# Kernel optimization log

Hardware: AMD Instinct MI355X
Metric: run time of the kernel (lower is better)

Reference implementation:

```python
import jax, jax.numpy as jnp
import numpy as np

B, S, E, H, L = 32, 1024, 768, 64, 2  # batch, seq (<=1024 per bias buffer), embed, head hidden, labels
MASKED_BIAS = jnp.float32(-10000.0)


def setup_inputs() -> dict:
    key = jax.random.key(0)
    ks = jax.random.split(key, 12)
    s = 0.02  # init scale
    return {
        "hidden": jax.random.normal(ks[0], (B, S, E), dtype=jnp.float32),
        "attention_mask": jnp.ones((B, S), dtype=jnp.float32),
        # torch nn.Linear weights are [out, in]
        "Wk": jax.random.normal(ks[1], (E, E), dtype=jnp.float32) * s,
        "bk": jnp.zeros((E,), dtype=jnp.float32),
        "Wq": jax.random.normal(ks[2], (E, E), dtype=jnp.float32) * s,
        "bq": jnp.zeros((E,), dtype=jnp.float32),
        "Wv": jax.random.normal(ks[3], (E, E), dtype=jnp.float32) * s,
        "bv": jnp.zeros((E,), dtype=jnp.float32),
        "W1": jax.random.normal(ks[4], (H, E), dtype=jnp.float32) * s,
        "b1": jnp.zeros((H,), dtype=jnp.float32),
        "W2": jax.random.normal(ks[5], (L, H), dtype=jnp.float32) * s,
        "b2": jnp.zeros((L,), dtype=jnp.float32),
    }


def reference(hidden, attention_mask, Wk, bk, Wq, bq, Wv, bv, W1, b1, W2, b2):
    # Single-head causal attention, NO 1/sqrt(d) scaling (faithful to source).
    # Dropout layers run in eval mode -> identity.
    seq = hidden.shape[1]
    q = hidden @ Wq.T + bq            # [B,S,E]
    k = hidden @ Wk.T + bk            # [B,S,E]
    v = hidden @ Wv.T + bv            # [B,S,E] (v_drop is identity in eval)
    w = jnp.einsum('bqe,bke->bqk', q, k)  # [B,S,S]
    causal = jnp.tril(jnp.ones((seq, seq), dtype=bool))  # bias[:, ns-nd:ns, :ns] with nd==ns
    w = jnp.where(causal, w, MASKED_BIAS.astype(w.dtype))
    am = (1.0 - attention_mask)[:, None, :] * -10000.0    # [B,1,S]
    w = jax.nn.softmax(w + am, axis=-1)
    h = jnp.einsum('bqk,bke->bqe', w, v)  # [B,S,E]
    h = jax.nn.relu(h @ W1.T + b1)        # [B,S,64]
    return h @ W2.T + b2                  # [B,S,L]
```

## Files before the change

kernel.cpp:

```cpp
#include <hip/hip_runtime.h>
#include <hip/hip_bf16.h>
#include <cstdio>


typedef _Float16 f16;
typedef f16    f16x8 __attribute__((ext_vector_type(8)));
typedef f16    f16x4 __attribute__((ext_vector_type(4)));
typedef __bf16 bfx8  __attribute__((ext_vector_type(8)));
typedef float  f32x4 __attribute__((ext_vector_type(4)));

#define MFMA_F16(a,b,c)  __builtin_amdgcn_mfma_f32_16x16x32_f16((a),(b),(c),0,0,0)
#define MFMA_BF16(a,b,c) __builtin_amdgcn_mfma_f32_16x16x32_bf16((a),(b),(c),0,0,0)

static constexpr int LDT2 = 264;

__device__ __forceinline__ void gl_lds16(const void* g, void* l) {
    __builtin_amdgcn_global_load_lds(
        (const __attribute__((address_space(1))) void*)g,
        (__attribute__((address_space(3))) void*)l, 16, 0, 0);
}

#define WAIT_VMCNT(n)                                        \
    do { asm volatile("s_waitcnt vmcnt(" #n ")");            \
         __builtin_amdgcn_sched_barrier(0); } while (0)
#define WAIT_LGKM0()                                         \
    do { asm volatile("s_waitcnt lgkmcnt(0)");               \
         __builtin_amdgcn_sched_barrier(0); } while (0)

__global__ __launch_bounds__(256) void cvt_all(
    const float* __restrict__ hidden,
    const float* __restrict__ Wq, const float* __restrict__ Wk, const float* __restrict__ Wv,
    f16* __restrict__ h16, f16* __restrict__ oq, f16* __restrict__ ok, f16* __restrict__ ov)
{
    const int bid = blockIdx.x;
    const float* src;
    f16* dst;
    int base;
    if (bid < 24576) {
        src = hidden; dst = h16;
        base = (bid * 256 + threadIdx.x) * 4;
    } else {
        int wz = (bid - 24576) / 576, wb = (bid - 24576) % 576;
        src = (wz == 0) ? Wq : (wz == 1) ? Wk : Wv;
        dst = (wz == 0) ? oq : (wz == 1) ? ok : ov;
        base = (wb * 256 + threadIdx.x) * 4;
    }
    f32x4 v = *(const f32x4*)(src + base);
    f16x4 o;
    #pragma unroll
    for (int e = 0; e < 4; ++e) o[e] = (f16)v[e];
    *(f16x4*)(dst + base) = o;
}

#define QPHASE(fr0, STAGE_STMT, GATE_STMT)                                        \
    {                                                                             \
        f16x8 afr[2][2];                                                          \
        _Pragma("unroll")                                                         \
        for (int i = 0; i < 2; ++i) {                                             \
            _Pragma("unroll")                                                     \
            for (int kk = 0; kk < 2; ++kk)                                        \
                afr[i][kk] = *(const f16x8*)&SA[kk * 8192 + (wr8 + (fr0) + i) * 512 + lq]; \
        }                                                                         \
        STAGE_STMT;                                                               \
        GATE_STMT;                                                                \
        __builtin_amdgcn_s_barrier();                                             \
        WAIT_LGKM0();                                                             \
        __builtin_amdgcn_s_setprio(1);                                            \
        _Pragma("unroll")                                                         \
        for (int i = 0; i < 2; ++i) {                                             \
            _Pragma("unroll")                                                     \
            for (int jj = 0; jj < 4; ++jj) {                                      \
                acc[(fr0) + i][jj] = MFMA_F16(afr[i][0], bfr[jj][0], acc[(fr0) + i][jj]); \
                acc[(fr0) + i][jj] = MFMA_F16(afr[i][1], bfr[jj][1], acc[(fr0) + i][jj]); \
            }                                                                     \
        }                                                                         \
        __builtin_amdgcn_s_setprio(0);                                            \
        __builtin_amdgcn_s_barrier();                                             \
    }

#define QPHASE_BF(fr0, STAGE_STMT, GATE_STMT)                                     \
    {                                                                             \
        bfx8 afr[2][2];                                                           \
        _Pragma("unroll")                                                         \
        for (int i = 0; i < 2; ++i) {                                             \
            _Pragma("unroll")                                                     \
            for (int kk = 0; kk < 2; ++kk)                                        \
                afr[i][kk] = *(const bfx8*)&SA[kk * 8192 + (wr8 + (fr0) + i) * 512 + lq]; \
        }                                                                         \
        STAGE_STMT;                                                               \
        GATE_STMT;                                                                \
        __builtin_amdgcn_s_barrier();                                             \
        WAIT_LGKM0();                                                             \
        __builtin_amdgcn_s_setprio(1);                                            \
        _Pragma("unroll")                                                         \
        for (int i = 0; i < 2; ++i) {                                             \
            _Pragma("unroll")                                                     \
            for (int jj = 0; jj < 4; ++jj) {                                      \
                acc[(fr0) + i][jj] = MFMA_BF16(afr[i][0], bfr[jj][0], acc[(fr0) + i][jj]); \
                acc[(fr0) + i][jj] = MFMA_BF16(afr[i][1], bfr[jj][1], acc[(fr0) + i][jj]); \
            }                                                                     \
        }                                                                         \
        __builtin_amdgcn_s_setprio(0);                                            \
        __builtin_amdgcn_s_barrier();                                             \
    }

__global__ __launch_bounds__(512, 2) void qkv_kernel(
    const f16* __restrict__ h16,
    const f16* __restrict__ wq, const f16* __restrict__ wk, const f16* __restrict__ wv,
    const float* __restrict__ bq, const float* __restrict__ bk, const float* __restrict__ bv,
    f16* __restrict__ q16, f16* __restrict__ k16, __bf16* __restrict__ vT)
{
    const int f = blockIdx.x;
    const int xcd = f & 7;
    const int j = f >> 3;
    const int nt = j % 3;
    const int z  = (j / 3) % 3;
    const int mi = j / 9;
    const int mt = xcd + 8 * mi;
    const int m0 = mt * 256, n0 = nt * 256;

    const f16* W = (z == 0) ? wq : (z == 1) ? wk : wv;
    const float* bias = (z == 0) ? bq : (z == 1) ? bk : bv;

    __shared__ alignas(16) f16 S[65536];

    const int t = threadIdx.x, lane = t & 63, wave = t >> 6;
    const int wr = wave >> 2, wc = wave & 3;
    const int wr8 = wr * 8;
    const int quad = lane >> 4, l16 = lane & 15;
    const int lq = quad * 128 + l16 * 8;

    const f16* gA = h16 + (size_t)(m0 + l16) * 768 + quad * 8;
    const f16* gB = W   + (size_t)(n0 + l16) * 768 + quad * 8;
    int gofs[2], lofs[2];
    #pragma unroll
    for (int u = 0; u < 2; ++u) {
        int unit = wave * 2 + u;
        int kk = unit >> 3, c = unit & 7;
        gofs[u] = c * 16 * 768 + kk * 32;
        lofs[u] = kk * 8192 + c * 512;
    }
    auto stage = [&](int kt, int mat, int half) {
        const f16* gp = (mat ? gB : gA) + half * (128 * 768) + kt * 64;
        f16* lp = &S[(kt & 1) * 32768 + mat * 16384 + half * 4096];
        gl_lds16(gp + gofs[0], lp + lofs[0]);
        gl_lds16(gp + gofs[1], lp + lofs[1]);
    };

    f32x4 acc[8][4] = {};

    stage(0, 0, 0); stage(0, 0, 1); stage(0, 1, 0); stage(0, 1, 1);
    stage(1, 1, 0); stage(1, 1, 1);
    WAIT_VMCNT(4);
    __builtin_amdgcn_s_barrier();

    f16x8 bfr[4][2];
    for (int kt = 0; kt < 12; ++kt) {
        const f16* SA = &S[(kt & 1) * 32768];
        const f16* SB = SA + 16384;
        #pragma unroll
        for (int jj = 0; jj < 4; ++jj) {
            #pragma unroll
            for (int kk = 0; kk < 2; ++kk)
                bfr[jj][kk] = *(const f16x8*)&SB[kk * 8192 + (wc * 4 + jj) * 512 + lq];
        }
        QPHASE(0, { if (kt + 1 < 12) stage(kt + 1, 0, 0); }, {});
        QPHASE(2, { if (kt + 1 < 12) stage(kt + 1, 0, 1); }, {});
        QPHASE(4, { if (kt + 2 < 12) stage(kt + 2, 1, 0); }, {});
        QPHASE(6, { if (kt + 2 < 12) stage(kt + 2, 1, 1); },
               {
                   if (kt + 2 < 12)       WAIT_VMCNT(4);
                   else if (kt + 1 < 12)  WAIT_VMCNT(0);
               });
    }

    if (z < 2) {
        f16* out = z ? k16 : q16;
        #pragma unroll
        for (int jj = 0; jj < 4; ++jj) {
            int col = n0 + wc * 64 + jj * 16 + l16;
            float bb = bias[col];
            #pragma unroll
            for (int fi = 0; fi < 8; ++fi) {
                #pragma unroll
                for (int r = 0; r < 4; ++r) {
                    int row = m0 + wr * 128 + fi * 16 + quad * 4 + r;
                    out[(size_t)row * 768 + col] = (f16)(acc[fi][jj][r] + bb);
                }
            }
        }
    } else {
        __bf16* Tb = (__bf16*)S;
        const int halfw = wc >> 1;
        const int bofs = (m0 >> 10) * 768;
        const int s0 = m0 & 1023;
        #pragma unroll
        for (int half = 0; half < 2; ++half) {
            __syncthreads();
            if (halfw == half) {
                #pragma unroll
                for (int jj = 0; jj < 4; ++jj) {
                    int el = (wc & 1) * 64 + jj * 16 + l16;
                    float bb = bias[n0 + half * 128 + el];
                    #pragma unroll
                    for (int fi = 0; fi < 8; ++fi) {
                        #pragma unroll
                        for (int r = 0; r < 4; ++r) {
                            int sl = wr * 128 + fi * 16 + quad * 4 + r;
                            Tb[el * LDT2 + sl] = (__bf16)(acc[fi][jj][r] + bb);
                        }
                    }
                }
            }
            __syncthreads();
            const int ch = (t & 31) * 8;
            const int rbase = t >> 5;
            #pragma unroll
            for (int p = 0; p < 8; ++p) {
                int e = rbase + p * 16;
                bfx8 val = *(const bfx8*)&Tb[e * LDT2 + ch];
                *(bfx8*)&vT[(size_t)(bofs + n0 + half * 128 + e) * 1024 + s0 + ch] = val;
            }
        }
    }
}

__global__ __launch_bounds__(512, 2) void logits_kernel(
    const f16* __restrict__ q16, const f16* __restrict__ k16,
    const float* __restrict__ amask, __bf16* __restrict__ pu, float* __restrict__ psum)
{
    const int f = blockIdx.x;
    const int xcd = f & 7;
    const int j = f >> 3;
    const int b = xcd + 8 * (j / 10);
    const int tile = j % 10;
    int mt, nt;
    if (tile < 4)      { mt = 3; nt = tile; }
    else if (tile < 7) { mt = 2; nt = tile - 4; }
    else if (tile < 9) { mt = 1; nt = tile - 7; }
    else               { mt = 0; nt = 0; }
    const int m0 = mt * 256, n0 = nt * 256;
    const size_t pb = (size_t)b << 20;
    const size_t qb = (size_t)b * 1024 * 768;

    __shared__ alignas(16) f16 S[65536];
    __shared__ float rs[4][256];

    const int t = threadIdx.x, lane = t & 63, wave = t >> 6;
    const int wr = wave >> 2, wc = wave & 3;
    const int wr8 = wr * 8;
    const int quad = lane >> 4, l16 = lane & 15;
    const int lq = quad * 128 + l16 * 8;

    const f16* gA = q16 + qb + (size_t)(m0 + l16) * 768 + quad * 8;
    const f16* gB = k16 + qb + (size_t)(n0 + l16) * 768 + quad * 8;
    int gofs[2], lofs[2];
    #pragma unroll
    for (int u = 0; u < 2; ++u) {
        int unit = wave * 2 + u;
        int kk = unit >> 3, c = unit & 7;
        gofs[u] = c * 16 * 768 + kk * 32;
        lofs[u] = kk * 8192 + c * 512;
    }
    auto stage = [&](int kt, int mat, int half) {
        const f16* gp = (mat ? gB : gA) + half * (128 * 768) + kt * 64;
        f16* lp = &S[(kt & 1) * 32768 + mat * 16384 + half * 4096];
        gl_lds16(gp + gofs[0], lp + lofs[0]);
        gl_lds16(gp + gofs[1], lp + lofs[1]);
    };

    f32x4 acc[8][4] = {};

    stage(0, 0, 0); stage(0, 0, 1); stage(0, 1, 0); stage(0, 1, 1);
    stage(1, 1, 0); stage(1, 1, 1);
    WAIT_VMCNT(4);
    __builtin_amdgcn_s_barrier();

    f16x8 bfr[4][2];
    for (int kt = 0; kt < 12; ++kt) {
        const f16* SA = &S[(kt & 1) * 32768];
        const f16* SB = SA + 16384;
        #pragma unroll
        for (int jj = 0; jj < 4; ++jj) {
            #pragma unroll
            for (int kk = 0; kk < 2; ++kk)
                bfr[jj][kk] = *(const f16x8*)&SB[kk * 8192 + (wc * 4 + jj) * 512 + lq];
        }
        QPHASE(0, { if (kt + 1 < 12) stage(kt + 1, 0, 0); }, {});
        QPHASE(2, { if (kt + 1 < 12) stage(kt + 1, 0, 1); }, {});
        QPHASE(4, { if (kt + 2 < 12) stage(kt + 2, 1, 0); }, {});
        QPHASE(6, { if (kt + 2 < 12) stage(kt + 2, 1, 1); },
               {
                   if (kt + 2 < 12)       WAIT_VMCNT(4);
                   else if (kt + 1 < 12)  WAIT_VMCNT(0);
               });
    }

    float rp[8][4] = {};
    #pragma unroll
    for (int jj = 0; jj < 4; ++jj) {
        int col = n0 + wc * 64 + jj * 16 + l16;
        float am = (1.0f - amask[b * 1024 + col]) * -10000.0f;
        #pragma unroll
        for (int fi = 0; fi < 8; ++fi) {
            #pragma unroll
            for (int r = 0; r < 4; ++r) {
                int row = m0 + wr * 128 + fi * 16 + quad * 4 + r;
                float s = acc[fi][jj][r] + am;
                float pval = (col <= row) ? __expf(fminf(s, 80.0f)) : 0.0f;
                pu[pb + (size_t)row * 1024 + col] = (__bf16)pval;
                rp[fi][r] += pval;
            }
        }
    }
    #pragma unroll
    for (int fi = 0; fi < 8; ++fi) {
        #pragma unroll
        for (int r = 0; r < 4; ++r) {
            float v = rp[fi][r];
            v += __shfl_xor(v, 1, 64);
            v += __shfl_xor(v, 2, 64);
            v += __shfl_xor(v, 4, 64);
            v += __shfl_xor(v, 8, 64);
            if (l16 == 0) rs[wc][wr * 128 + fi * 16 + quad * 4 + r] = v;
        }
    }
    __syncthreads();
    if (t < 256)
        psum[((size_t)b * 1024 + m0 + t) * 4 + nt] =
            rs[0][t] + rs[1][t] + rs[2][t] + rs[3][t];
}

__global__ __launch_bounds__(512, 2) void pv_kernel(
    const __bf16* __restrict__ pu, const __bf16* __restrict__ vT,
    const float* __restrict__ psum, __bf16* __restrict__ h)
{
    const int f = blockIdx.x;
    const int xcd = f & 7;
    const int j = f >> 3;
    const int b = xcd + 8 * (j / 12);
    const int tile = j % 12;
    const int mt = 3 - tile / 3, nt = tile % 3;
    const int m0 = mt * 256, n0 = nt * 256;
    const int nkt = 4 * (mt + 1);
    const size_t pb = (size_t)b << 20;
    const size_t vb = (size_t)b * 768 * 1024;

    __shared__ alignas(16) __bf16 S[65536];
    __shared__ float invl[256];

    const int t = threadIdx.x, lane = t & 63, wave = t >> 6;
    const int wr = wave >> 2, wc = wave & 3;
    const int wr8 = wr * 8;
    const int quad = lane >> 4, l16 = lane & 15;
    const int lq = quad * 128 + l16 * 8;

    if (t < 256) {
        int row = m0 + t;
        int lim = row >> 8;
        const float* pr = &psum[((size_t)b * 1024 + row) * 4];
        float s = 0.f;
        #pragma unroll
        for (int n = 0; n < 4; ++n) s += (n <= lim) ? pr[n] : 0.f;
        invl[t] = 1.0f / s;
    }

    const __bf16* gA = pu + pb + (size_t)(m0 + l16) * 1024 + quad * 8;
    const __bf16* gB = vT + vb + (size_t)(n0 + l16) * 1024 + quad * 8;
    int gofs[2], lofs[2];
    #pragma unroll
    for (int u = 0; u < 2; ++u) {
        int unit = wave * 2 + u;
        int kk = unit >> 3, c = unit & 7;
        gofs[u] = c * 16 * 1024 + kk * 32;
        lofs[u] = kk * 8192 + c * 512;
    }
    auto stage = [&](int kt, int mat, int half) {
        const __bf16* gp = (mat ? gB : gA) + half * (128 * 1024) + kt * 64;
        __bf16* lp = &S[(kt & 1) * 32768 + mat * 16384 + half * 4096];
        gl_lds16(gp + gofs[0], lp + lofs[0]);
        gl_lds16(gp + gofs[1], lp + lofs[1]);
    };

    f32x4 acc[8][4] = {};

    stage(0, 0, 0); stage(0, 0, 1); stage(0, 1, 0); stage(0, 1, 1);
    stage(1, 1, 0); stage(1, 1, 1);
    WAIT_VMCNT(4);
    __builtin_amdgcn_s_barrier();

    bfx8 bfr[4][2];
    for (int kt = 0; kt < nkt; ++kt) {
        const __bf16* SA = &S[(kt & 1) * 32768];
        const __bf16* SB = SA + 16384;
        #pragma unroll
        for (int jj = 0; jj < 4; ++jj) {
            #pragma unroll
            for (int kk = 0; kk < 2; ++kk)
                bfr[jj][kk] = *(const bfx8*)&SB[kk * 8192 + (wc * 4 + jj) * 512 + lq];
        }
        QPHASE_BF(0, { if (kt + 1 < nkt) stage(kt + 1, 0, 0); }, {});
        QPHASE_BF(2, { if (kt + 1 < nkt) stage(kt + 1, 0, 1); }, {});
        QPHASE_BF(4, { if (kt + 2 < nkt) stage(kt + 2, 1, 0); }, {});
        QPHASE_BF(6, { if (kt + 2 < nkt) stage(kt + 2, 1, 1); },
               {
                   if (kt + 2 < nkt)       WAIT_VMCNT(4);
                   else if (kt + 1 < nkt)  WAIT_VMCNT(0);
               });
    }

    #pragma unroll
    for (int jj = 0; jj < 4; ++jj) {
        int col = n0 + wc * 64 + jj * 16 + l16;
        #pragma unroll
        for (int fi = 0; fi < 8; ++fi) {
            #pragma unroll
            for (int r = 0; r < 4; ++r) {
                int rl = wr * 128 + fi * 16 + quad * 4 + r;
                h[((size_t)b * 1024 + m0 + rl) * 768 + col] = (__bf16)(acc[fi][jj][r] * invl[rl]);
            }
        }
    }
}

__global__ __launch_bounds__(256) void mlp_kernel(
    const __bf16* __restrict__ h, const float* __restrict__ W1, const float* __restrict__ b1,
    const float* __restrict__ W2, const float* __restrict__ b2, float* __restrict__ out)
{
    const int wave = threadIdx.x >> 6, lane = threadIdx.x & 63;
    const int quad = lane >> 4, l16 = lane & 15;
    const int m0 = blockIdx.x * 64 + wave * 16;

    f32x4 acc[4] = {};
    for (int k0 = 0; k0 < 768; k0 += 32) {
        bfx8 af = *(const bfx8*)&h[(size_t)(m0 + l16) * 768 + k0 + quad * 8];
        #pragma unroll
        for (int jj = 0; jj < 4; ++jj) {
            const float* wp = W1 + (size_t)(jj * 16 + l16) * 768 + k0 + quad * 8;
            f32x4 w0 = *(const f32x4*)wp;
            f32x4 w1 = *(const f32x4*)(wp + 4);
            bfx8 bg;
            #pragma unroll
            for (int e = 0; e < 4; ++e) { bg[e] = (__bf16)w0[e]; bg[e + 4] = (__bf16)w1[e]; }
            acc[jj] = MFMA_BF16(af, bg, acc[jj]);
        }
    }
    float part[4][2] = {};
    #pragma unroll
    for (int jj = 0; jj < 4; ++jj) {
        int c = jj * 16 + l16;
        float bb = b1[c];
        float w20 = W2[c], w21 = W2[64 + c];
        #pragma unroll
        for (int r = 0; r < 4; ++r) {
            float x = fmaxf(acc[jj][r] + bb, 0.f);
            part[r][0] += x * w20;
            part[r][1] += x * w21;
        }
    }
    #pragma unroll
    for (int off = 1; off < 16; off <<= 1)
        #pragma unroll
        for (int r = 0; r < 4; ++r) {
            part[r][0] += __shfl_xor(part[r][0], off, 64);
            part[r][1] += __shfl_xor(part[r][1], off, 64);
        }
    if (l16 == 0) {
        #pragma unroll
        for (int r = 0; r < 4; ++r) {
            int row = m0 + quad * 4 + r;
            out[(size_t)row * 2 + 0] = part[r][0] + b2[0];
            out[(size_t)row * 2 + 1] = part[r][1] + b2[1];
        }
    }
}

extern "C" void kernel_launch(void* const* d_in, const int* in_sizes, int n_in,
                              void* d_out, int out_size, void* d_ws, size_t ws_size,
                              hipStream_t stream)
{
    const float* hidden = (const float*)d_in[0];
    const float* amask  = (const float*)d_in[1];
    const float* Wk = (const float*)d_in[2];
    const float* bk = (const float*)d_in[3];
    const float* Wq = (const float*)d_in[4];
    const float* bq = (const float*)d_in[5];
    const float* Wv = (const float*)d_in[6];
    const float* bv = (const float*)d_in[7];
    const float* W1 = (const float*)d_in[8];
    const float* b1 = (const float*)d_in[9];
    const float* W2 = (const float*)d_in[10];
    const float* b2 = (const float*)d_in[11];
    float* out = (float*)d_out;

    char* ws = (char*)d_ws;
    const size_t MB = 1024 * 1024;
    f16* h16 = (f16*)ws;
    f16* wq16 = (f16*)(ws + 48 * MB);
    f16* wk16 = wq16 + 589824;
    f16* wv16 = wk16 + 589824;
    __bf16* pu  = (__bf16*)ws;
    float*  psum = (float*)(ws + 64 * MB);
    f16* q16 = (f16*)(ws + 66 * MB);
    f16* k16 = (f16*)(ws + 114 * MB);
    __bf16* vT = (__bf16*)(ws + 162 * MB);
    __bf16* h  = (__bf16*)(ws + 66 * MB);
    const size_t NEED = 210 * MB;
    if (ws_size < NEED) {
        fprintf(stderr, "[Attn kernel] ws too small: %zu < %zu — skipping launches\n",
                ws_size, NEED);
        return;
    }

    cvt_all<<<24576 + 1728, 256, 0, stream>>>(
        hidden, Wq, Wk, Wv, h16, wq16, wk16, wv16);

    qkv_kernel<<<1152, 512, 0, stream>>>(
        h16, wq16, wk16, wv16, bq, bk, bv, q16, k16, vT);
    logits_kernel<<<320, 512, 0, stream>>>(q16, k16, amask, pu, psum);
    pv_kernel<<<384, 512, 0, stream>>>(pu, vT, psum, h);
    mlp_kernel<<<512, 256, 0, stream>>>(h, W1, b1, W2, b2, out);
}
```

Measured before the change: 519.5 us.

## Replace direct global-to-LDS loads with register-staged prefetch in all GEMM kernels

```diff
diff --git a/kernel.cpp b/kernel.cpp
--- a/kernel.cpp
+++ b/kernel.cpp
@@ -8,23 +8,16 @@
 typedef f16    f16x4 __attribute__((ext_vector_type(4)));
 typedef __bf16 bfx8  __attribute__((ext_vector_type(8)));
 typedef float  f32x4 __attribute__((ext_vector_type(4)));
+typedef unsigned int u32;
+typedef u32    u32x4 __attribute__((ext_vector_type(4)));
 
 #define MFMA_F16(a,b,c)  __builtin_amdgcn_mfma_f32_16x16x32_f16((a),(b),(c),0,0,0)
 #define MFMA_BF16(a,b,c) __builtin_amdgcn_mfma_f32_16x16x32_bf16((a),(b),(c),0,0,0)
 
 static constexpr int LDT2 = 264;
 
-__device__ __forceinline__ void gl_lds16(const void* g, void* l) {
-    __builtin_amdgcn_global_load_lds(
-        (const __attribute__((address_space(1))) void*)g,
-        (__attribute__((address_space(3))) void*)l, 16, 0, 0);
-}
-
-#define WAIT_VMCNT(n)                                        \
-    do { asm volatile("s_waitcnt vmcnt(" #n ")");            \
-         __builtin_amdgcn_sched_barrier(0); } while (0)
-#define WAIT_LGKM0()                                         \
-    do { asm volatile("s_waitcnt lgkmcnt(0)");               \
+#define PUB()                                                \
+    do { asm volatile("s_waitcnt lgkmcnt(0)" ::: "memory");  \
          __builtin_amdgcn_sched_barrier(0); } while (0)
 
 __global__ __launch_bounds__(256) void cvt_all(
@@ -52,19 +45,19 @@
     *(f16x4*)(dst + base) = o;
 }
 
-#define QPHASE(fr0, STAGE_STMT, GATE_STMT)                                        \
+#define QPHASE(fr0, ST_STMT, LD_STMT)                                             \
     {                                                                             \
         f16x8 afr[2][2];                                                          \
         _Pragma("unroll")                                                         \
         for (int i = 0; i < 2; ++i) {                                             \
             _Pragma("unroll")                                                     \
-            for (int kk = 0; kk < 2; ++kk)                                        \
-                afr[i][kk] = *(const f16x8*)&SA[kk * 8192 + (wr8 + (fr0) + i) * 512 + lq]; \
+            for (int kk2 = 0; kk2 < 2; ++kk2)                                     \
+                afr[i][kk2] = *(const f16x8*)&SA[kk2 * 8192 + (wr8 + (fr0) + i) * 512 + lq]; \
         }                                                                         \
-        STAGE_STMT;                                                               \
-        GATE_STMT;                                                                \
+        ST_STMT;                                                                  \
+        LD_STMT;                                                                  \
+        PUB();                                                                    \
         __builtin_amdgcn_s_barrier();                                             \
-        WAIT_LGKM0();                                                             \
         __builtin_amdgcn_s_setprio(1);                                            \
         _Pragma("unroll")                                                         \
         for (int i = 0; i < 2; ++i) {                                             \
@@ -78,19 +71,19 @@
         __builtin_amdgcn_s_barrier();                                             \
     }
 
-#define QPHASE_BF(fr0, STAGE_STMT, GATE_STMT)                                     \
+#define QPHASE_BF(fr0, ST_STMT, LD_STMT)                                          \
     {                                                                             \
         bfx8 afr[2][2];                                                           \
         _Pragma("unroll")                                                         \
         for (int i = 0; i < 2; ++i) {                                             \
             _Pragma("unroll")                                                     \
-            for (int kk = 0; kk < 2; ++kk)                                        \
-                afr[i][kk] = *(const bfx8*)&SA[kk * 8192 + (wr8 + (fr0) + i) * 512 + lq]; \
+            for (int kk2 = 0; kk2 < 2; ++kk2)                                     \
+                afr[i][kk2] = *(const bfx8*)&SA[kk2 * 8192 + (wr8 + (fr0) + i) * 512 + lq]; \
         }                                                                         \
-        STAGE_STMT;                                                               \
-        GATE_STMT;                                                                \
+        ST_STMT;                                                                  \
+        LD_STMT;                                                                  \
+        PUB();                                                                    \
         __builtin_amdgcn_s_barrier();                                             \
-        WAIT_LGKM0();                                                             \
         __builtin_amdgcn_s_setprio(1);                                            \
         _Pragma("unroll")                                                         \
         for (int i = 0; i < 2; ++i) {                                             \
@@ -103,6 +96,15 @@
         __builtin_amdgcn_s_setprio(0);                                            \
         __builtin_amdgcn_s_barrier();                                             \
     }
+
+#define LD2(s_a, s_b, GP)                                    \
+    do { const char* _g = (const char*)(GP);                 \
+         s_a = *(const u32x4*)_g;                            \
+         s_b = *(const u32x4*)(_g + GO1B); } while (0)
+#define ST2(s_a, s_b, LP)                                    \
+    do { char* _l = (char*)(LP);                             \
+         *(u32x4*)_l = s_a;                                  \
+         *(u32x4*)(_l + 1024) = s_b; } while (0)
 
 __global__ __launch_bounds__(512, 2) void qkv_kernel(
     const f16* __restrict__ h16,
@@ -130,29 +132,34 @@
     const int quad = lane >> 4, l16 = lane & 15;
     const int lq = quad * 128 + l16 * 8;
 
-    const f16* gA = h16 + (size_t)(m0 + l16) * 768 + quad * 8;
-    const f16* gB = W   + (size_t)(n0 + l16) * 768 + quad * 8;
-    int gofs[2], lofs[2];
-    #pragma unroll
-    for (int u = 0; u < 2; ++u) {
-        int unit = wave * 2 + u;
-        int kk = unit >> 3, c = unit & 7;
-        gofs[u] = c * 16 * 768 + kk * 32;
-        lofs[u] = kk * 8192 + c * 512;
-    }
-    auto stage = [&](int kt, int mat, int half) {
-        const f16* gp = (mat ? gB : gA) + half * (128 * 768) + kt * 64;
-        f16* lp = &S[(kt & 1) * 32768 + mat * 16384 + half * 4096];
-        gl_lds16(gp + gofs[0], lp + lofs[0]);
-        gl_lds16(gp + gofs[1], lp + lofs[1]);
+    enum { GO1B = 16 * 768 * 2, HOFF = 128 * 768 };
+    const int c0 = (wave * 2) & 7, kk0 = wave >> 2;
+    const int gofs0 = c0 * 16 * 768 + kk0 * 32;
+    const int lofs0 = kk0 * 8192 + c0 * 512 + lane * 8;
+
+    const f16* gA = h16 + (size_t)(m0 + l16) * 768 + quad * 8 + gofs0;
+    const f16* gB = W   + (size_t)(n0 + l16) * 768 + quad * 8 + gofs0;
+    auto gp = [&](int mat, int kt, int half) {
+        return (mat ? gB : gA) + half * HOFF + kt * 64;
     };
+    auto lp = [&](int kt, int mat, int half) {
+        return &S[(kt & 1) * 32768 + mat * 16384 + half * 4096 + lofs0];
+    };
 
     f32x4 acc[8][4] = {};
-
-    stage(0, 0, 0); stage(0, 0, 1); stage(0, 1, 0); stage(0, 1, 1);
-    stage(1, 1, 0); stage(1, 1, 1);
-    WAIT_VMCNT(4);
-    __builtin_amdgcn_s_barrier();
+    u32x4 sA0a, sA0b, sA1a, sA1b, sB0a, sB0b, sB1a, sB1b;
+
+    {
+        u32x4 p0a, p0b, p1a, p1b, p2a, p2b, p3a, p3b, p4a, p4b, p5a, p5b;
+        LD2(p0a, p0b, gp(0, 0, 0)); LD2(p1a, p1b, gp(0, 0, 1));
+        LD2(p2a, p2b, gp(1, 0, 0)); LD2(p3a, p3b, gp(1, 0, 1));
+        LD2(p4a, p4b, gp(1, 1, 0)); LD2(p5a, p5b, gp(1, 1, 1));
+        ST2(p0a, p0b, lp(0, 0, 0)); ST2(p1a, p1b, lp(0, 0, 1));
+        ST2(p2a, p2b, lp(0, 1, 0)); ST2(p3a, p3b, lp(0, 1, 1));
+        ST2(p4a, p4b, lp(1, 1, 0)); ST2(p5a, p5b, lp(1, 1, 1));
+        PUB();
+        __builtin_amdgcn_s_barrier();
+    }
 
     f16x8 bfr[4][2];
     for (int kt = 0; kt < 12; ++kt) {
@@ -161,17 +168,17 @@
         #pragma unroll
         for (int jj = 0; jj < 4; ++jj) {
             #pragma unroll
-            for (int kk = 0; kk < 2; ++kk)
-                bfr[jj][kk] = *(const f16x8*)&SB[kk * 8192 + (wc * 4 + jj) * 512 + lq];
-        }
-        QPHASE(0, { if (kt + 1 < 12) stage(kt + 1, 0, 0); }, {});
-        QPHASE(2, { if (kt + 1 < 12) stage(kt + 1, 0, 1); }, {});
-        QPHASE(4, { if (kt + 2 < 12) stage(kt + 2, 1, 0); }, {});
-        QPHASE(6, { if (kt + 2 < 12) stage(kt + 2, 1, 1); },
-               {
-                   if (kt + 2 < 12)       WAIT_VMCNT(4);
-                   else if (kt + 1 < 12)  WAIT_VMCNT(0);
-               });
+            for (int kk2 = 0; kk2 < 2; ++kk2)
+                bfr[jj][kk2] = *(const f16x8*)&SB[kk2 * 8192 + (wc * 4 + jj) * 512 + lq];
+        }
+        QPHASE(0, { if (kt > 0 && kt + 1 < 12) ST2(sB0a, sB0b, lp(kt + 1, 1, 0)); },
+                  { if (kt + 1 < 12) LD2(sA0a, sA0b, gp(0, kt + 1, 0)); });
+        QPHASE(2, { if (kt > 0 && kt + 1 < 12) ST2(sB1a, sB1b, lp(kt + 1, 1, 1)); },
+                  { if (kt + 1 < 12) LD2(sA1a, sA1b, gp(0, kt + 1, 1)); });
+        QPHASE(4, { if (kt + 1 < 12) ST2(sA0a, sA0b, lp(kt + 1, 0, 0)); },
+                  { if (kt + 2 < 12) LD2(sB0a, sB0b, gp(1, kt + 2, 0)); });
+        QPHASE(6, { if (kt + 1 < 12) ST2(sA1a, sA1b, lp(kt + 1, 0, 1)); },
+                  { if (kt + 2 < 12) LD2(sB1a, sB1b, gp(1, kt + 2, 1)); });
     }
 
     if (z < 2) {
@@ -252,29 +259,34 @@
     const int quad = lane >> 4, l16 = lane & 15;
     const int lq = quad * 128 + l16 * 8;
 
-    const f16* gA = q16 + qb + (size_t)(m0 + l16) * 768 + quad * 8;
-    const f16* gB = k16 + qb + (size_t)(n0 + l16) * 768 + quad * 8;
-    int gofs[2], lofs[2];
-    #pragma unroll
-    for (int u = 0; u < 2; ++u) {
-        int unit = wave * 2 + u;
-        int kk = unit >> 3, c = unit & 7;
-        gofs[u] = c * 16 * 768 + kk * 32;
-        lofs[u] = kk * 8192 + c * 512;
-    }
-    auto stage = [&](int kt, int mat, int half) {
-        const f16* gp = (mat ? gB : gA) + half * (128 * 768) + kt * 64;
-        f16* lp = &S[(kt & 1) * 32768 + mat * 16384 + half * 4096];
-        gl_lds16(gp + gofs[0], lp + lofs[0]);
-        gl_lds16(gp + gofs[1], lp + lofs[1]);
+    enum { GO1B = 16 * 768 * 2, HOFF = 128 * 768 };
+    const int c0 = (wave * 2) & 7, kk0 = wave >> 2;
+    const int gofs0 = c0 * 16 * 768 + kk0 * 32;
+    const int lofs0 = kk0 * 8192 + c0 * 512 + lane * 8;
+
+    const f16* gA = q16 + qb + (size_t)(m0 + l16) * 768 + quad * 8 + gofs0;
+    const f16* gB = k16 + qb + (size_t)(n0 + l16) * 768 + quad * 8 + gofs0;
+    auto gp = [&](int mat, int kt, int half) {
+        return (mat ? gB : gA) + half * HOFF + kt * 64;
     };
+    auto lp = [&](int kt, int mat, int half) {
+        return &S[(kt & 1) * 32768 + mat * 16384 + half * 4096 + lofs0];
+    };
 
     f32x4 acc[8][4] = {};
-
-    stage(0, 0, 0); stage(0, 0, 1); stage(0, 1, 0); stage(0, 1, 1);
-    stage(1, 1, 0); stage(1, 1, 1);
-    WAIT_VMCNT(4);
-    __builtin_amdgcn_s_barrier();
+    u32x4 sA0a, sA0b, sA1a, sA1b, sB0a, sB0b, sB1a, sB1b;
+
+    {
+        u32x4 p0a, p0b, p1a, p1b, p2a, p2b, p3a, p3b, p4a, p4b, p5a, p5b;
+        LD2(p0a, p0b, gp(0, 0, 0)); LD2(p1a, p1b, gp(0, 0, 1));
+        LD2(p2a, p2b, gp(1, 0, 0)); LD2(p3a, p3b, gp(1, 0, 1));
+        LD2(p4a, p4b, gp(1, 1, 0)); LD2(p5a, p5b, gp(1, 1, 1));
+        ST2(p0a, p0b, lp(0, 0, 0)); ST2(p1a, p1b, lp(0, 0, 1));
+        ST2(p2a, p2b, lp(0, 1, 0)); ST2(p3a, p3b, lp(0, 1, 1));
+        ST2(p4a, p4b, lp(1, 1, 0)); ST2(p5a, p5b, lp(1, 1, 1));
+        PUB();
+        __builtin_amdgcn_s_barrier();
+    }
 
     f16x8 bfr[4][2];
     for (int kt = 0; kt < 12; ++kt) {
@@ -283,17 +295,17 @@
         #pragma unroll
         for (int jj = 0; jj < 4; ++jj) {
             #pragma unroll
-            for (int kk = 0; kk < 2; ++kk)
-                bfr[jj][kk] = *(const f16x8*)&SB[kk * 8192 + (wc * 4 + jj) * 512 + lq];
-        }
-        QPHASE(0, { if (kt + 1 < 12) stage(kt + 1, 0, 0); }, {});
-        QPHASE(2, { if (kt + 1 < 12) stage(kt + 1, 0, 1); }, {});
-        QPHASE(4, { if (kt + 2 < 12) stage(kt + 2, 1, 0); }, {});
-        QPHASE(6, { if (kt + 2 < 12) stage(kt + 2, 1, 1); },
-               {
-                   if (kt + 2 < 12)       WAIT_VMCNT(4);
-                   else if (kt + 1 < 12)  WAIT_VMCNT(0);
-               });
+            for (int kk2 = 0; kk2 < 2; ++kk2)
+                bfr[jj][kk2] = *(const f16x8*)&SB[kk2 * 8192 + (wc * 4 + jj) * 512 + lq];
+        }
+        QPHASE(0, { if (kt > 0 && kt + 1 < 12) ST2(sB0a, sB0b, lp(kt + 1, 1, 0)); },
+                  { if (kt + 1 < 12) LD2(sA0a, sA0b, gp(0, kt + 1, 0)); });
+        QPHASE(2, { if (kt > 0 && kt + 1 < 12) ST2(sB1a, sB1b, lp(kt + 1, 1, 1)); },
+                  { if (kt + 1 < 12) LD2(sA1a, sA1b, gp(0, kt + 1, 1)); });
+        QPHASE(4, { if (kt + 1 < 12) ST2(sA0a, sA0b, lp(kt + 1, 0, 0)); },
+                  { if (kt + 2 < 12) LD2(sB0a, sB0b, gp(1, kt + 2, 0)); });
+        QPHASE(6, { if (kt + 1 < 12) ST2(sA1a, sA1b, lp(kt + 1, 0, 1)); },
+                  { if (kt + 2 < 12) LD2(sB1a, sB1b, gp(1, kt + 2, 1)); });
     }
 
     float rp[8][4] = {};
@@ -365,29 +377,34 @@
         invl[t] = 1.0f / s;
     }
 
-    const __bf16* gA = pu + pb + (size_t)(m0 + l16) * 1024 + quad * 8;
-    const __bf16* gB = vT + vb + (size_t)(n0 + l16) * 1024 + quad * 8;
-    int gofs[2], lofs[2];
-    #pragma unroll
-    for (int u = 0; u < 2; ++u) {
-        int unit = wave * 2 + u;
-        int kk = unit >> 3, c = unit & 7;
-        gofs[u] = c * 16 * 1024 + kk * 32;
-        lofs[u] = kk * 8192 + c * 512;
-    }
-    auto stage = [&](int kt, int mat, int half) {
-        const __bf16* gp = (mat ? gB : gA) + half * (128 * 1024) + kt * 64;
-        __bf16* lp = &S[(kt & 1) * 32768 + mat * 16384 + half * 4096];
-        gl_lds16(gp + gofs[0], lp + lofs[0]);
-        gl_lds16(gp + gofs[1], lp + lofs[1]);
+    enum { GO1B = 16 * 1024 * 2, HOFF = 128 * 1024 };
+    const int c0 = (wave * 2) & 7, kk0 = wave >> 2;
+    const int gofs0 = c0 * 16 * 1024 + kk0 * 32;
+    const int lofs0 = kk0 * 8192 + c0 * 512 + lane * 8;
+
+    const __bf16* gA = pu + pb + (size_t)(m0 + l16) * 1024 + quad * 8 + gofs0;
+    const __bf16* gB = vT + vb + (size_t)(n0 + l16) * 1024 + quad * 8 + gofs0;
+    auto gp = [&](int mat, int kt, int half) {
+        return (mat ? gB : gA) + half * HOFF + kt * 64;
     };
+    auto lp = [&](int kt, int mat, int half) {
+        return &S[(kt & 1) * 32768 + mat * 16384 + half * 4096 + lofs0];
+    };
 
     f32x4 acc[8][4] = {};
-
-    stage(0, 0, 0); stage(0, 0, 1); stage(0, 1, 0); stage(0, 1, 1);
-    stage(1, 1, 0); stage(1, 1, 1);
-    WAIT_VMCNT(4);
-    __builtin_amdgcn_s_barrier();
+    u32x4 sA0a, sA0b, sA1a, sA1b, sB0a, sB0b, sB1a, sB1b;
+
+    {
+        u32x4 p0a, p0b, p1a, p1b, p2a, p2b, p3a, p3b, p4a, p4b, p5a, p5b;
+        LD2(p0a, p0b, gp(0, 0, 0)); LD2(p1a, p1b, gp(0, 0, 1));
+        LD2(p2a, p2b, gp(1, 0, 0)); LD2(p3a, p3b, gp(1, 0, 1));
+        LD2(p4a, p4b, gp(1, 1, 0)); LD2(p5a, p5b, gp(1, 1, 1));
+        ST2(p0a, p0b, lp(0, 0, 0)); ST2(p1a, p1b, lp(0, 0, 1));
+        ST2(p2a, p2b, lp(0, 1, 0)); ST2(p3a, p3b, lp(0, 1, 1));
+        ST2(p4a, p4b, lp(1, 1, 0)); ST2(p5a, p5b, lp(1, 1, 1));
+        PUB();
+        __builtin_amdgcn_s_barrier();
+    }
 
     bfx8 bfr[4][2];
     for (int kt = 0; kt < nkt; ++kt) {
@@ -396,17 +413,17 @@
         #pragma unroll
         for (int jj = 0; jj < 4; ++jj) {
             #pragma unroll
-            for (int kk = 0; kk < 2; ++kk)
-                bfr[jj][kk] = *(const bfx8*)&SB[kk * 8192 + (wc * 4 + jj) * 512 + lq];
-        }
-        QPHASE_BF(0, { if (kt + 1 < nkt) stage(kt + 1, 0, 0); }, {});
-        QPHASE_BF(2, { if (kt + 1 < nkt) stage(kt + 1, 0, 1); }, {});
-        QPHASE_BF(4, { if (kt + 2 < nkt) stage(kt + 2, 1, 0); }, {});
-        QPHASE_BF(6, { if (kt + 2 < nkt) stage(kt + 2, 1, 1); },
-               {
-                   if (kt + 2 < nkt)       WAIT_VMCNT(4);
-                   else if (kt + 1 < nkt)  WAIT_VMCNT(0);
-               });
+            for (int kk2 = 0; kk2 < 2; ++kk2)
+                bfr[jj][kk2] = *(const bfx8*)&SB[kk2 * 8192 + (wc * 4 + jj) * 512 + lq];
+        }
+        QPHASE_BF(0, { if (kt > 0 && kt + 1 < nkt) ST2(sB0a, sB0b, lp(kt + 1, 1, 0)); },
+                     { if (kt + 1 < nkt) LD2(sA0a, sA0b, gp(0, kt + 1, 0)); });
+        QPHASE_BF(2, { if (kt > 0 && kt + 1 < nkt) ST2(sB1a, sB1b, lp(kt + 1, 1, 1)); },
+                     { if (kt + 1 < nkt) LD2(sA1a, sA1b, gp(0, kt + 1, 1)); });
+        QPHASE_BF(4, { if (kt + 1 < nkt) ST2(sA0a, sA0b, lp(kt + 1, 0, 0)); },
+                     { if (kt + 2 < nkt) LD2(sB0a, sB0b, gp(1, kt + 2, 0)); });
+        QPHASE_BF(6, { if (kt + 1 < nkt) ST2(sA1a, sA1b, lp(kt + 1, 0, 1)); },
+                     { if (kt + 2 < nkt) LD2(sB1a, sB1b, gp(1, kt + 2, 1)); });
     }
 
     #pragma unroll
```

New measurement: 529.6 us. No clear change (+2.0%).
